# Performance work log

Hardware: AMD Instinct MI355X
Metric: run time of the kernel (lower is better)

## Reference

```python
import jax, jax.numpy as jnp
import numpy as np

N, M, D_IN, D_K = 2048, 1024, 128, 64


def setup_inputs() -> dict:
    key = jax.random.key(0)
    kq, kk, kw = jax.random.split(key, 3)
    q = jax.random.normal(kq, (N, D_IN), dtype=jnp.float32)
    k = jax.random.normal(kk, (M, D_IN), dtype=jnp.float32)
    # glorot-uniform init for the bias-free Linear(d_in -> d_k) weight [d_k, d_in]
    limit = np.sqrt(6.0 / (D_IN + D_K)).astype(np.float32)
    W = jax.random.uniform(kw, (D_K, D_IN), dtype=jnp.float32, minval=-limit, maxval=limit)
    return {"q": q, "k": k, "W": W}


def reference(q, k, W):
    # pairwise broadcast difference: [n, m, d_in]
    diff = q[:, None, :] - k[None, :, :]
    # linear projection (nn.Linear: x @ W.T): [n, m, d_k]
    proj = jnp.einsum("nmd,kd->nmk", diff, W)
    # L2 norm over last dim: [n, m]
    dist = jnp.sqrt(jnp.sum(proj * proj, axis=-1))
    score = -dist * 0.5
    # masked_softmax with mask=None over dim=-1 == plain softmax over m
    return jax.nn.softmax(score, axis=-1)
```

## Files before the change

### kernel.cpp

```cpp
#include <hip/hip_runtime.h>
#include <math.h>

#define N_Q 2048
#define M_K 1024
#define DIN 128
#define DK  64

__global__ __launch_bounds__(256) void proj_kernel(
    const float* __restrict__ q, const float* __restrict__ k,
    const float* __restrict__ W, float* __restrict__ Qp,
    float* __restrict__ KpT, float* __restrict__ qn2, float* __restrict__ kn2)
{
    __shared__ float W_lds[DK][DIN + 4];
    __shared__ float row_lds[4][DIN];
    const int tx = threadIdx.x;

    const float4* W4 = (const float4*)W;
    #pragma unroll
    for (int i = 0; i < 8; ++i) {
        int idx = tx + i * 256;
        float4 v = W4[idx];
        int r = idx >> 5, c = (idx & 31) * 4;
        *(float4*)&W_lds[r][c] = v;
    }

    const int wave = tx >> 6, lane = tx & 63;
    const int row  = blockIdx.x * 4 + wave;
    const float* src = (row < N_Q) ? (q + (size_t)row * DIN)
                                   : (k + (size_t)(row - N_Q) * DIN);
    row_lds[wave][lane]      = src[lane];
    row_lds[wave][lane + 64] = src[lane + 64];
    __syncthreads();

    float acc = 0.f;
    #pragma unroll
    for (int d = 0; d < DIN; d += 4) {
        float4 wv = *(const float4*)&W_lds[lane][d];
        float4 rv = *(const float4*)&row_lds[wave][d];
        acc = fmaf(wv.x, rv.x, acc);
        acc = fmaf(wv.y, rv.y, acc);
        acc = fmaf(wv.z, rv.z, acc);
        acc = fmaf(wv.w, rv.w, acc);
    }

    float sq = acc * acc;
    #pragma unroll
    for (int off = 32; off >= 1; off >>= 1)
        sq += __shfl_xor(sq, off, 64);

    if (row < N_Q) {
        Qp[(size_t)row * DK + lane] = acc;
        if (lane == 0) qn2[row] = sq;
    } else {
        const int m = row - N_Q;
        KpT[(size_t)lane * M_K + m] = acc;
        if (lane == 0) kn2[m] = sq;
    }
}

__global__ __launch_bounds__(512) void score_kernel(
    const float* __restrict__ Qp, const float* __restrict__ KpT,
    const float* __restrict__ qn2, const float* __restrict__ kn2,
    float* __restrict__ out)
{
    __shared__ float qpT[DK][8];
    __shared__ float qn2s[8];
    __shared__ float redmax[8][8];
    __shared__ float redsum[8][8];

    const int tx = threadIdx.x;
    const int n0 = blockIdx.x * 8;
    const int wave = tx >> 6, lane = tx & 63;

    {
        int r = tx & 7, d = tx >> 3;
        qpT[d][r] = Qp[(size_t)(n0 + r) * DK + d];
        if (tx < 8) qn2s[tx] = qn2[n0 + tx];
    }
    __syncthreads();

    float acc[8][2];
    #pragma unroll
    for (int r = 0; r < 8; ++r) { acc[r][0] = 0.f; acc[r][1] = 0.f; }

    const float2* K2 = (const float2*)KpT;
    #pragma unroll 8
    for (int d = 0; d < DK; ++d) {
        float2 kv = K2[d * (M_K / 2) + tx];
        float4 qa = *(const float4*)&qpT[d][0];
        float4 qb = *(const float4*)&qpT[d][4];
        float qv[8] = {qa.x, qa.y, qa.z, qa.w, qb.x, qb.y, qb.z, qb.w};
        #pragma unroll
        for (int r = 0; r < 8; ++r) {
            acc[r][0] = fmaf(qv[r], kv.x, acc[r][0]);
            acc[r][1] = fmaf(qv[r], kv.y, acc[r][1]);
        }
    }

    float2 kv2 = ((const float2*)kn2)[tx];
    float kn2a[2] = {kv2.x, kv2.y};
    #pragma unroll
    for (int r = 0; r < 8; ++r) {
        float qn = qn2s[r];
        #pragma unroll
        for (int i = 0; i < 2; ++i) {
            float d2 = fmaxf(fmaf(-2.f, acc[r][i], qn + kn2a[i]), 0.f);
            acc[r][i] = -0.5f * sqrtf(d2);
        }
    }

    #pragma unroll
    for (int r = 0; r < 8; ++r) {
        float m = fmaxf(acc[r][0], acc[r][1]);
        #pragma unroll
        for (int off = 32; off >= 1; off >>= 1)
            m = fmaxf(m, __shfl_xor(m, off, 64));
        if (lane == 0) redmax[r][wave] = m;
    }
    __syncthreads();

    float mx[8];
    #pragma unroll
    for (int r = 0; r < 8; ++r) {
        float4 a = *(const float4*)&redmax[r][0];
        float4 b = *(const float4*)&redmax[r][4];
        mx[r] = fmaxf(fmaxf(fmaxf(a.x, a.y), fmaxf(a.z, a.w)),
                      fmaxf(fmaxf(b.x, b.y), fmaxf(b.z, b.w)));
    }

    #pragma unroll
    for (int r = 0; r < 8; ++r) {
        acc[r][0] = __expf(acc[r][0] - mx[r]);
        acc[r][1] = __expf(acc[r][1] - mx[r]);
        float t = acc[r][0] + acc[r][1];
        #pragma unroll
        for (int off = 32; off >= 1; off >>= 1)
            t += __shfl_xor(t, off, 64);
        if (lane == 0) redsum[r][wave] = t;
    }
    __syncthreads();

    #pragma unroll
    for (int r = 0; r < 8; ++r) {
        float4 a = *(const float4*)&redsum[r][0];
        float4 b = *(const float4*)&redsum[r][4];
        float total = (a.x + a.y + a.z + a.w) + (b.x + b.y + b.z + b.w);
        float inv = 1.0f / total;
        float2 o = make_float2(acc[r][0] * inv, acc[r][1] * inv);
        ((float2*)out)[(size_t)(n0 + r) * (M_K / 2) + tx] = o;
    }
}

extern "C" void kernel_launch(void* const* d_in, const int* in_sizes, int n_in,
                              void* d_out, int out_size, void* d_ws, size_t ws_size,
                              hipStream_t stream)
{
    const float* q = (const float*)d_in[0];
    const float* k = (const float*)d_in[1];
    const float* W = (const float*)d_in[2];
    float* out = (float*)d_out;

    float* Qp  = (float*)d_ws;
    float* KpT = Qp + (size_t)N_Q * DK;
    float* qn2 = KpT + (size_t)DK * M_K;
    float* kn2 = qn2 + N_Q;

    proj_kernel<<<(N_Q + M_K) / 4, 256, 0, stream>>>(q, k, W, Qp, KpT, qn2, kn2);
    score_kernel<<<N_Q / 8, 512, 0, stream>>>(Qp, KpT, qn2, kn2, out);
}
```

Before: 22.97 us.

## Compute projection with split-bf16 MFMA using few large blocks

Replaces the scalar FP32 projection kernel with a matrix-core version. Inputs and weights are split into bf16 high and low parts, and three bf16 MFMA products approximate FP32 precision. Each wave handles 16 rows, and only 24 blocks of 512 threads are launched, so W is loaded once per block instead of once per 4 rows. The cost is conversion overhead, slightly reduced precision from the 3-term split, and low occupancy from launching only 24 blocks.

Result: no change. 23.28 us (+1.4%).

```diff
diff --git a/kernel.cpp b/kernel.cpp
--- a/kernel.cpp
+++ b/kernel.cpp
@@ -1,4 +1,5 @@
 #include <hip/hip_runtime.h>
+#include <hip/hip_bf16.h>
 #include <math.h>
 
 #define N_Q 2048
@@ -6,55 +7,123 @@
 #define DIN 128
 #define DK  64
 
-__global__ __launch_bounds__(256) void proj_kernel(
+typedef __attribute__((ext_vector_type(8))) short short8;
+typedef __attribute__((ext_vector_type(4))) float f32x4;
+
+static __device__ __forceinline__ void split8(const float* v, short8& h, short8& l)
+{
+    __attribute__((aligned(16))) unsigned int hu[4], lu[4];
+    #pragma unroll
+    for (int i = 0; i < 4; ++i) {
+        __hip_bfloat16 h0 = __float2bfloat16(v[2*i]);
+        __hip_bfloat16 h1 = __float2bfloat16(v[2*i+1]);
+        float f0 = __bfloat162float(h0), f1 = __bfloat162float(h1);
+        __hip_bfloat16 l0 = __float2bfloat16(v[2*i]   - f0);
+        __hip_bfloat16 l1 = __float2bfloat16(v[2*i+1] - f1);
+        hu[i] = (unsigned)*(unsigned short*)&h0 | ((unsigned)*(unsigned short*)&h1 << 16);
+        lu[i] = (unsigned)*(unsigned short*)&l0 | ((unsigned)*(unsigned short*)&l1 << 16);
+    }
+    h = *(short8*)hu;
+    l = *(short8*)lu;
+}
+
+__global__ __launch_bounds__(512) void proj_mfma_kernel(
     const float* __restrict__ q, const float* __restrict__ k,
-    const float* __restrict__ W, float* __restrict__ Qp,
-    float* __restrict__ KpT, float* __restrict__ qn2, float* __restrict__ kn2)
-{
-    __shared__ float W_lds[DK][DIN + 4];
-    __shared__ float row_lds[4][DIN];
+    const float* __restrict__ W,
+    float* __restrict__ Qp, float* __restrict__ KpT,
+    float* __restrict__ qn2, float* __restrict__ kn2)
+{
+    __shared__ __align__(16) unsigned char smem[34816];
+
     const int tx = threadIdx.x;
-
-    const float4* W4 = (const float4*)W;
-    #pragma unroll
-    for (int i = 0; i < 8; ++i) {
-        int idx = tx + i * 256;
-        float4 v = W4[idx];
-        int r = idx >> 5, c = (idx & 31) * 4;
-        *(float4*)&W_lds[r][c] = v;
-    }
-
-    const int wave = tx >> 6, lane = tx & 63;
-    const int row  = blockIdx.x * 4 + wave;
+    const int w = tx >> 6, lane = tx & 63;
+    const int g = lane >> 4, c = lane & 15;
+
+    {
+        const float4* W4 = (const float4*)W;
+        float4* Wst = (float4*)smem;
+        #pragma unroll
+        for (int i = 0; i < 4; ++i) Wst[tx + 512*i] = W4[tx + 512*i];
+    }
+    __syncthreads();
+
+    {
+        __attribute__((aligned(16))) float wreg[16];
+        #pragma unroll
+        for (int i = 0; i < 4; ++i)
+            *(float4*)(wreg + 4*i) = ((float4*)smem)[4*tx + i];
+        __syncthreads();
+        short8 h0, l0, h1, l1;
+        split8(wreg, h0, l0);
+        split8(wreg + 8, h1, l1);
+        const int r = tx >> 3, c0 = (tx & 7) * 16;
+        unsigned short* Wh = (unsigned short*)smem;
+        unsigned short* Wl = (unsigned short*)(smem + 17408);
+        *(short8*)&Wh[r*136 + c0]     = h0;
+        *(short8*)&Wh[r*136 + c0 + 8] = h1;
+        *(short8*)&Wl[r*136 + c0]     = l0;
+        *(short8*)&Wl[r*136 + c0 + 8] = l1;
+    }
+    __syncthreads();
+
+    short8 WAh[4][4], WAl[4][4];
+    {
+        const unsigned short* Wh = (const unsigned short*)smem;
+        const unsigned short* Wl = (const unsigned short*)(smem + 17408);
+        #pragma unroll
+        for (int og = 0; og < 4; ++og)
+            #pragma unroll
+            for (int ks = 0; ks < 4; ++ks) {
+                WAh[og][ks] = *(const short8*)&Wh[(16*og + c)*136 + 32*ks + 8*g];
+                WAl[og][ks] = *(const short8*)&Wl[(16*og + c)*136 + 32*ks + 8*g];
+            }
+    }
+
+    const int t = blockIdx.x * 8 + w;
+    const int row = 16*t + c;
     const float* src = (row < N_Q) ? (q + (size_t)row * DIN)
                                    : (k + (size_t)(row - N_Q) * DIN);
-    row_lds[wave][lane]      = src[lane];
-    row_lds[wave][lane + 64] = src[lane + 64];
-    __syncthreads();
-
-    float acc = 0.f;
-    #pragma unroll
-    for (int d = 0; d < DIN; d += 4) {
-        float4 wv = *(const float4*)&W_lds[lane][d];
-        float4 rv = *(const float4*)&row_lds[wave][d];
-        acc = fmaf(wv.x, rv.x, acc);
-        acc = fmaf(wv.y, rv.y, acc);
-        acc = fmaf(wv.z, rv.z, acc);
-        acc = fmaf(wv.w, rv.w, acc);
-    }
-
-    float sq = acc * acc;
-    #pragma unroll
-    for (int off = 32; off >= 1; off >>= 1)
-        sq += __shfl_xor(sq, off, 64);
+
+    f32x4 qa[4];
+    #pragma unroll
+    for (int og = 0; og < 4; ++og) qa[og] = (f32x4){0.f,0.f,0.f,0.f};
+
+    #pragma unroll
+    for (int ks = 0; ks < 4; ++ks) {
+        __attribute__((aligned(16))) float rv[8];
+        *(float4*)rv       = *(const float4*)(src + 32*ks + 8*g);
+        *(float4*)(rv + 4) = *(const float4*)(src + 32*ks + 8*g + 4);
+        short8 bh, bl;
+        split8(rv, bh, bl);
+        #pragma unroll
+        for (int og = 0; og < 4; ++og) {
+            qa[og] = __builtin_amdgcn_mfma_f32_16x16x32_bf16(WAh[og][ks], bh, qa[og], 0,0,0);
+            qa[og] = __builtin_amdgcn_mfma_f32_16x16x32_bf16(WAh[og][ks], bl, qa[og], 0,0,0);
+            qa[og] = __builtin_amdgcn_mfma_f32_16x16x32_bf16(WAl[og][ks], bh, qa[og], 0,0,0);
+        }
+    }
+
+    float nrm = 0.f;
+    #pragma unroll
+    for (int og = 0; og < 4; ++og)
+        #pragma unroll
+        for (int j = 0; j < 4; ++j) nrm += qa[og][j]*qa[og][j];
+    nrm += __shfl_xor(nrm, 16, 64);
+    nrm += __shfl_xor(nrm, 32, 64);
 
     if (row < N_Q) {
-        Qp[(size_t)row * DK + lane] = acc;
-        if (lane == 0) qn2[row] = sq;
+        #pragma unroll
+        for (int og = 0; og < 4; ++og)
+            *(float4*)&Qp[(size_t)row * DK + 16*og + 4*g] = *(float4*)&qa[og];
+        if (g == 0) qn2[row] = nrm;
     } else {
         const int m = row - N_Q;
-        KpT[(size_t)lane * M_K + m] = acc;
-        if (lane == 0) kn2[m] = sq;
+        #pragma unroll
+        for (int og = 0; og < 4; ++og)
+            #pragma unroll
+            for (int j = 0; j < 4; ++j)
+                KpT[(size_t)(16*og + 4*g + j) * M_K + m] = qa[og][j];
+        if (g == 0) kn2[m] = nrm;
     }
 }
 
@@ -160,11 +229,12 @@
     const float* W = (const float*)d_in[2];
     float* out = (float*)d_out;
 
-    float* Qp  = (float*)d_ws;
-    float* KpT = Qp + (size_t)N_Q * DK;
-    float* qn2 = KpT + (size_t)DK * M_K;
-    float* kn2 = qn2 + N_Q;
-
-    proj_kernel<<<(N_Q + M_K) / 4, 256, 0, stream>>>(q, k, W, Qp, KpT, qn2, kn2);
+    unsigned char* base = (unsigned char*)d_ws;
+    float* Qp  = (float*)base;
+    float* KpT = (float*)(base + 524288);
+    float* qn2 = (float*)(base + 786432);
+    float* kn2 = (float*)(base + 794624);
+
+    proj_mfma_kernel<<<24, 512, 0, stream>>>(q, k, W, Qp, KpT, qn2, kn2);
     score_kernel<<<N_Q / 8, 512, 0, stream>>>(Qp, KpT, qn2, kn2, out);
 }
```
